# Kernel optimization log

Hardware: AMD Instinct MI355X
Metric: run time of the kernel (lower is better)

The kernel has to match this reference:

```python
import jax, jax.numpy as jnp
import numpy as np

SEQ, B, V, E, H, L = 64, 64, 32000, 512, 512, 2


def setup_inputs() -> dict:
    key = jax.random.key(0)
    ks = jax.random.split(key, 12)
    k = float(np.sqrt(1.0 / H))
    u = lambda kk, shape, a, b: jax.random.uniform(kk, shape, jnp.float32, a, b)
    return {
        "inputs": jax.random.randint(ks[0], (SEQ, B), 0, V),          # [T, B] token ids
        "hidden": jnp.zeros((L, B, H), jnp.float32),                   # initial hidden
        "emb": u(ks[1], (V, E), -0.1, 0.1),                            # embedding table
        "Wr_w": u(ks[2], (L, H, E + H), -k, k),                        # reset gate [L,H,2H]
        "Wr_b": u(ks[3], (L, H), -k, k),
        "Wz_w": u(ks[4], (L, H, E + H), -k, k),                        # update gate
        "Wz_b": u(ks[5], (L, H), -k, k),
        "Wh_w": u(ks[6], (L, H, E + H), -k, k),                        # candidate
        "Wh_b": u(ks[7], (L, H), -k, k),
        "out_w": u(ks[8], (V, H), -0.1, 0.1),                          # output projection
        "out_b": jnp.zeros((V,), jnp.float32),
    }


def reference(inputs, hidden, emb, Wr_w, Wr_b, Wz_w, Wz_b, Wh_w, Wh_b, out_w, out_b):
    # GRU recurrence over time via lax.scan (dropout disabled: dp_keep_prob=1.0)
    def step(h, tok):
        x = emb[tok]  # [B, E]
        new_h = []
        for i in range(L):  # fixed small layer loop
            hi = h[i]  # [B, H]
            cat = jnp.concatenate([x, hi], axis=1)  # [B, E+H]
            r = jax.nn.sigmoid(cat @ Wr_w[i].T + Wr_b[i])
            z = jax.nn.sigmoid(cat @ Wz_w[i].T + Wz_b[i])
            h_hat = jnp.tanh(jnp.concatenate([x, r * hi], axis=1) @ Wh_w[i].T + Wh_b[i])
            x = (1.0 - z) * hi + z * h_hat  # next layer input / new hidden
            new_h.append(x)
        logits_t = x @ out_w.T + out_b  # [B, V]
        return jnp.stack(new_h), logits_t

    hidden_final, logits = jax.lax.scan(step, hidden, inputs)
    return logits, hidden_final  # [T,B,V], [L,B,H]
```

## Files before the change

kernel.cpp:

```cpp
#include <hip/hip_runtime.h>

constexpr int NT = 64;
constexpr int NB = 64;
constexpr int NV = 32000;
constexpr int NE = 512;
constexpr int NH = 512;
constexpr int NTILE = 32 * 250;

constexpr size_t SZ_OW  = (size_t)NV * NE;
constexpr size_t SZ_XE  = (size_t)NT * NB * NE;
constexpr size_t SZ_H   = (size_t)NB * NH;
constexpr size_t LOGITS = (size_t)NT * NB * NV;

typedef float f32x4 __attribute__((ext_vector_type(4)));
typedef int   i32x4 __attribute__((ext_vector_type(4)));
typedef short bf16x8 __attribute__((ext_vector_type(8)));
typedef short s16x4 __attribute__((ext_vector_type(4)));
typedef _Float16 f16x8 __attribute__((ext_vector_type(8)));

__device__ __forceinline__ unsigned short f2bf(float x) {
  unsigned u = __float_as_uint(x);
  u += 0x7FFFu + ((u >> 16) & 1u);
  return (unsigned short)(u >> 16);
}
__device__ __forceinline__ float bf2f(unsigned short s) {
  return __uint_as_float(((unsigned)s) << 16);
}
__device__ __forceinline__ void split2(float v, short* hi, short* lo) {
  unsigned short h = f2bf(v);
  *hi = (short)h;
  *lo = (short)f2bf(v - bf2f(h));
}
__device__ __forceinline__ f32x4 mma_bf16(bf16x8 a, bf16x8 b, f32x4 c) {
  return __builtin_amdgcn_mfma_f32_16x16x32_bf16(a, b, c, 0, 0, 0);
}
__device__ __forceinline__ f32x4 mma_f16(f16x8 a, f16x8 b, f32x4 c) {
  return __builtin_amdgcn_mfma_f32_16x16x32_f16(a, b, c, 0, 0, 0);
}

__device__ __forceinline__ void st_sc32u(unsigned* p, unsigned v) {
  asm volatile("global_store_dword %0, %1, off sc0 sc1" :: "v"(p), "v"(v) : "memory");
}
__device__ __forceinline__ void st_sc128(void* p, i32x4 v) {
  asm volatile("global_store_dwordx4 %0, %1, off sc0 sc1" :: "v"(p), "v"(v) : "memory");
}
__device__ __forceinline__ void st_nt(float* p, float v) {
  asm volatile("global_store_dword %0, %1, off nt" :: "v"(p), "v"(v) : "memory");
}
__device__ __forceinline__ unsigned ld_sc32u(const unsigned* p) {
  unsigned v;
  asm volatile("global_load_dword %0, %1, off sc0 sc1\n\ts_waitcnt vmcnt(0)"
               : "=v"(v) : "v"(p) : "memory");
  return v;
}

__device__ __forceinline__ void publish(unsigned* flags, int slot, unsigned val) {
  asm volatile("s_waitcnt vmcnt(0)" ::: "memory");
  __syncthreads();
  if (threadIdx.x == 0) st_sc32u(&flags[(size_t)slot * 32], val);
}

__global__ void k_prep(
    const float* __restrict__ outw, const int* __restrict__ toks,
    const float* __restrict__ emb, const float* __restrict__ hid,
    _Float16* OWf, short* XeHi, short* XeLo,
    short* X1Hi, short* X1Lo, short* h0Hi, short* h0Lo) {
  const size_t stride = (size_t)gridDim.x * blockDim.x;
  const size_t N1 = SZ_OW, N2 = N1 + SZ_XE, N3 = N2 + SZ_H, N4 = N3 + SZ_H;
  for (size_t x = (size_t)blockIdx.x * blockDim.x + threadIdx.x; x < N4; x += stride) {
    if (x < N1) {
      OWf[x] = (_Float16)outw[x];
    } else if (x < N2) {
      size_t p = x - N1;
      size_t r = p >> 9, c = p & 511u;
      int tok = toks[r];
      float v = emb[(size_t)tok * 512 + c];
      short hi, lo; split2(v, &hi, &lo);
      XeHi[p] = hi; XeLo[p] = lo;
    } else if (x < N3) {
      size_t p = x - N2;
      short hi, lo; split2(hid[p], &hi, &lo);
      h0Hi[p] = hi; h0Lo[p] = lo;
    } else {
      size_t p = x - N3;
      short hi, lo; split2(hid[SZ_H + p], &hi, &lo);
      X1Hi[p] = hi; X1Lo[p] = lo;
    }
  }
}

__device__ __forceinline__ void mmaP32(
    const short* __restrict__ aH, const short* __restrict__ aL, int base,
    const short* lsHi_, const short* lsLo_,
    f32x4 (&accH)[2], f32x4 (&accL)[2], int wave, int l15, int lq) {
  const int kq = wave >> 1, rhalf = wave & 1;
  const int r0 = rhalf * 16 + l15;
#pragma unroll
  for (int i = 0; i < 4; ++i) {
    const int ko = kq * 128 + i * 32 + lq * 8;
    const int kg = base + ko;
    const int e0 = (l15 * 1024 + kg) ^ ((l15 & 7) << 3);
    const int e1 = ((16 + l15) * 1024 + kg) ^ ((l15 & 7) << 3);
    bf16x8 bh0 = *(const bf16x8*)&lsHi_[e0];
    bf16x8 bl0 = *(const bf16x8*)&lsLo_[e0];
    bf16x8 bh1 = *(const bf16x8*)&lsHi_[e1];
    bf16x8 bl1 = *(const bf16x8*)&lsLo_[e1];
    bf16x8 ah = *(const bf16x8*)&aH[r0 * 512 + ko];
    bf16x8 al = *(const bf16x8*)&aL[r0 * 512 + ko];
    accH[0] = mma_bf16(ah, bh0, accH[0]);
    accH[1] = mma_bf16(ah, bh1, accH[1]);
    accL[0] = mma_bf16(al, bh0, accL[0]);
    accL[1] = mma_bf16(al, bh1, accL[1]);
    accL[0] = mma_bf16(ah, bl0, accL[0]);
    accL[1] = mma_bf16(ah, bl1, accL[1]);
  }
}
__device__ __forceinline__ void reduce4(float* lsRed_, f32x4 (&accH)[2], f32x4 (&accL)[2],
                                        f32x4 (&acc)[2], int wave, int l15, int lq) {
  const int kq = wave >> 1, rhalf = wave & 1;
  acc[0] = accH[0] + accL[0];
  acc[1] = accH[1] + accL[1];
  const int pos = l15 * 16 + lq * 4;
  if (kq) {
    *(f32x4*)&lsRed_[(((kq - 1) * 2 + rhalf) * 2 + 0) * 256 + pos] = acc[0];
    *(f32x4*)&lsRed_[(((kq - 1) * 2 + rhalf) * 2 + 1) * 256 + pos] = acc[1];
  }
  __syncthreads();
  if (!kq) {
#pragma unroll
    for (int s = 0; s < 3; ++s) {
      acc[0] += *(const f32x4*)&lsRed_[((s * 2 + rhalf) * 2 + 0) * 256 + pos];
      acc[1] += *(const f32x4*)&lsRed_[((s * 2 + rhalf) * 2 + 1) * 256 + pos];
    }
  }
  __syncthreads();
}

__device__ __forceinline__ void mmaD(
    const short* __restrict__ pAH, const short* __restrict__ pAL,
    int kloc0, int kkGlob0, const short* lsHi_, const short* lsLo_,
    f32x4 (&accH)[2], f32x4 (&accL)[2], int l15, int lq, int rhalf, int rowbase) {
  const int r0 = rowbase + rhalf * 16 + l15;
#pragma unroll 4
  for (int i = 0; i < 8; ++i) {
    const int kk = kkGlob0 + i * 32 + lq * 8;
    const int ka = kloc0 + i * 32 + lq * 8;
    const int e0 = (l15 * 1024 + kk) ^ ((l15 & 7) << 3);
    const int e1 = ((16 + l15) * 1024 + kk) ^ ((l15 & 7) << 3);
    bf16x8 bh0 = *(const bf16x8*)&lsHi_[e0];
    bf16x8 bl0 = *(const bf16x8*)&lsLo_[e0];
    bf16x8 bh1 = *(const bf16x8*)&lsHi_[e1];
    bf16x8 bl1 = *(const bf16x8*)&lsLo_[e1];
    bf16x8 ah = *(const bf16x8*)&pAH[r0 * 512 + ka];
    bf16x8 al = *(const bf16x8*)&pAL[r0 * 512 + ka];
    accH[0] = mma_bf16(ah, bh0, accH[0]);
    accH[1] = mma_bf16(ah, bh1, accH[1]);
    accL[0] = mma_bf16(al, bh0, accL[0]);
    accL[1] = mma_bf16(al, bh1, accL[1]);
    accL[0] = mma_bf16(ah, bl0, accL[0]);
    accL[1] = mma_bf16(ah, bl1, accL[1]);
  }
}
__device__ __forceinline__ void phaseD(
    const short* aLoH, const short* aLoL,
    const short* aHiH, const short* aHiL,
    const short* lsHi_, const short* lsLo_, float* lsRed_,
    f32x4 (&acc)[2], int wave, int l15, int lq, int rowbase) {
  const int khalf = wave >> 1, rhalf = wave & 1;
  f32x4 accH[2] = {}, accL[2] = {};
  const short* pAH = (khalf < 2) ? aLoH : aHiH;
  const short* pAL = (khalf < 2) ? aLoL : aHiL;
  mmaD(pAH, pAL, (khalf & 1) * 256, khalf * 256, lsHi_, lsLo_,
       accH, accL, l15, lq, rhalf, rowbase);
  acc[0] = accH[0] + accL[0];
  acc[1] = accH[1] + accL[1];
  const int pos = l15 * 16 + lq * 4;
  if (wave >= 2) {
    *(f32x4*)&lsRed_[((wave - 2) * 2 + 0) * 256 + pos] = acc[0];
    *(f32x4*)&lsRed_[((wave - 2) * 2 + 1) * 256 + pos] = acc[1];
  }
  __syncthreads();
  if (wave < 2) {
#pragma unroll
    for (int s = 0; s < 3; ++s) {
      const int slot = (wave & 1) + 2 * s;
      acc[0] += *(const f32x4*)&lsRed_[(slot * 2 + 0) * 256 + pos];
      acc[1] += *(const f32x4*)&lsRed_[(slot * 2 + 1) * 256 + pos];
    }
  }
  __syncthreads();
}

__device__ __forceinline__ void stage_weights(
    short* lsHi, short* lsLo, const float* srcBase0, const float* srcBase1,
    int jc, int tid) {
  for (int i = tid; i < 8192; i += 512) {
    const int j = i >> 8;
    const int k4 = (i & 255) << 2;
    const int g = jc + j;
    const float* src = (srcBase1 && g >= 512)
        ? (srcBase1 + (size_t)(g - 512) * 1024 + k4)
        : (srcBase0 + (size_t)g * 1024 + k4);
    f32x4 v = *(const f32x4*)src;
    s16x4 h4, l4;
#pragma unroll
    for (int q = 0; q < 4; ++q) { short hi, lo; split2(v[q], &hi, &lo); h4[q] = hi; l4[q] = lo; }
    const int els = (j * 1024 + k4) ^ ((j & 7) << 3);
    *(s16x4*)&lsHi[els] = h4;
    *(s16x4*)&lsLo[els] = l4;
  }
}

__device__ void gemm_loop(char* pool, int tid,
                          const _Float16* Af, const _Float16* Bw,
                          const float* bias, float* C,
                          unsigned* flags, unsigned* tcnt) {
  _Float16* lsA = (_Float16*)pool;
  _Float16* lsB = lsA + 128 * 64;
  volatile int* bc = (volatile int*)(pool + 32768);
  const int wave = tid >> 6, lane = tid & 63, l15 = lane & 15, lq = lane >> 4;
  const int wr = (wave >> 2) * 64, wc = (wave & 3) * 32;
  unsigned lastR = 0;
  __syncthreads();
  for (;;) {
    if (tid == 0)
      *bc = (int)__hip_atomic_fetch_add(tcnt, 1u, __ATOMIC_RELAXED,
                                        __HIP_MEMORY_SCOPE_AGENT);
    __syncthreads();
    const int tau = *bc;
    __syncthreads();
    if (tau >= NTILE) break;
    const int bm = tau / 250, bn = tau - bm * 250;
    const unsigned Rneed = 2u * (unsigned)bm + 2u;
    if (lastR < Rneed) {
      if (tid < 32) {
        const unsigned* fp = &flags[(size_t)(160 + tid) * 32];
        while (ld_sc32u(fp) < Rneed) __builtin_amdgcn_s_sleep(8);
      }
      lastR = Rneed;
    }
    __syncthreads();
    f32x4 acc[4][2] = {};
    const size_t arow0 = (size_t)bm * 128;
    const size_t brow0 = (size_t)bn * 128;
    for (int kb = 0; kb < 512; kb += 64) {
#pragma unroll
      for (int i = 0; i < 2; ++i) {
        int c = tid + i * 512;
        int row = c >> 3, kc = (c & 7) * 8;
        f16x8 va = *(const f16x8*)(Af + (arow0 + row) * 512 + kb + kc);
        f16x8 vb = *(const f16x8*)(Bw + (brow0 + row) * 512 + kb + kc);
        int el = (row * 64 + kc) ^ ((row & 7) << 3);
        *(f16x8*)&lsA[el] = va;
        *(f16x8*)&lsB[el] = vb;
      }
      __syncthreads();
#pragma unroll
      for (int k0 = 0; k0 < 64; k0 += 32) {
        const int kk = k0 + lq * 8;
        f16x8 af[4], bfr[2];
#pragma unroll
        for (int i = 0; i < 4; ++i) {
          int ra = wr + i * 16 + l15;
          af[i] = *(const f16x8*)&lsA[(ra * 64 + kk) ^ ((ra & 7) << 3)];
        }
#pragma unroll
        for (int jt = 0; jt < 2; ++jt) {
          int rb = wc + jt * 16 + l15;
          bfr[jt] = *(const f16x8*)&lsB[(rb * 64 + kk) ^ ((rb & 7) << 3)];
        }
#pragma unroll
        for (int i = 0; i < 4; ++i)
#pragma unroll
          for (int jt = 0; jt < 2; ++jt)
            acc[i][jt] = mma_f16(af[i], bfr[jt], acc[i][jt]);
      }
      __syncthreads();
    }
#pragma unroll
    for (int i = 0; i < 4; ++i) {
#pragma unroll
      for (int jt = 0; jt < 2; ++jt) {
        const size_t col = brow0 + wc + jt * 16 + l15;
        const float bval = bias[col];
#pragma unroll
        for (int r = 0; r < 4; ++r) {
          const size_t row = arow0 + wr + i * 16 + lq * 4 + r;
          st_nt(&C[row * (size_t)NV + col], acc[i][jt][r] + bval);
        }
      }
    }
  }
}

__launch_bounds__(512, 1)
__global__ void k_main(
    const float* __restrict__ Wr, const float* __restrict__ Wz, const float* __restrict__ Wh,
    const float* __restrict__ Wrb, const float* __restrict__ Wzb, const float* __restrict__ Whb,
    const short* __restrict__ XeHi, const short* __restrict__ XeLo,
    short* X1Hi, short* X1Lo, _Float16* X1f16,
    short* h0Hi, short* h0Lo,
    short* rh0Hi, short* rh0Lo, short* rh1Hi, short* rh1Lo,
    float* z0, float* z1, float* hidOut,
    const _Float16* OWf, const float* outb, float* out,
    unsigned* flags, unsigned* tcnt) {
  __shared__ __align__(16) char pool[153600];
  short* lsHi = (short*)pool;
  short* lsLo = lsHi + 32 * 1024;
  float* lsRed = (float*)(pool + 131072);
  short* sH    = (short*)(pool + 131072);
  short* sL    = sH + 1024;
  float* sZA   = (float*)(pool + 131072);
  short* stH   = (short*)(pool + 143360);
  short* stL   = stH + 1024;
  float* sZ    = (float*)(pool + 147456);
  _Float16* sX = (_Float16*)(pool + 151552);

  const int wg = blockIdx.x;
  const int tid = threadIdx.x;
  const int wave = tid >> 6, lane = tid & 63, l15 = lane & 15, lq = lane >> 4;

  if (wg < 64) {
    const int cg = wg >> 1, rh = wg & 1, jc = cg * 32, rowbase = rh * 32;
    const bool isR = (jc < 512);
    stage_weights(lsHi, lsLo, Wr, Wz, jc, tid);
    float biasL0, biasL1;
    {
      const int j0 = jc + l15, j1 = j0 + 16;
      biasL0 = (j0 < 512) ? Wrb[j0] : Wzb[j0 - 512];
      biasL1 = (j1 < 512) ? Wrb[j1] : Wzb[j1 - 512];
    }
    __syncthreads();
    for (int t = 0; t < NT; ++t) {
      f32x4 accH[2] = {}, accL[2] = {};
      mmaP32(XeHi + (size_t)t * SZ_H + rowbase * 512,
             XeLo + (size_t)t * SZ_H + rowbase * 512, 0,
             lsHi, lsLo, accH, accL, wave, l15, lq);
      if (tid < 16) {
        const unsigned* fp = &flags[(size_t)(128 + tid * 2 + rh) * 32];
        while (ld_sc32u(fp) < (unsigned)t) {}
      }
      __syncthreads();
      const short* hH = h0Hi + (size_t)t * SZ_H + rowbase * 512;
      const short* hL = h0Lo + (size_t)t * SZ_H + rowbase * 512;
      if (isR && tid < 256) {
        const int buf = tid >> 7, q = tid & 127, row = q >> 2, c = q & 3;
        *(i32x4*)&(buf ? stL : stH)[row * 32 + c * 8] =
            *(const i32x4*)((buf ? hL : hH) + row * 512 + jc + c * 8);
      }
      mmaP32(hH, hL, 512, lsHi, lsLo, accH, accL, wave, l15, lq);
      f32x4 acc[2];
      reduce4(lsRed, accH, accL, acc, wave, l15, lq);
      if (wave < 2) {
#pragma unroll
        for (int ct = 0; ct < 2; ++ct) {
          const int jj = ct * 16 + l15;
          const float bv = ct ? biasL1 : biasL0;
#pragma unroll
          for (int r = 0; r < 4; ++r) {
            const int lb = wave * 16 + lq * 4 + r;
            const float s = 1.0f / (1.0f + __expf(-(acc[ct][r] + bv)));
            if (isR) {
              const float hv = bf2f((unsigned short)stH[lb * 32 + jj]) +
                               bf2f((unsigned short)stL[lb * 32 + jj]);
              short hi, lo; split2(s * hv, &hi, &lo);
              sH[lb * 32 + jj] = hi; sL[lb * 32 + jj] = lo;
            } else {
              sZA[lb * 32 + jj] = s;
            }
          }
        }
      }
      __syncthreads();
      if (isR) {
        if (tid < 256) {
          const int buf = tid >> 7, q = tid & 127, row = q >> 2, c = q & 3;
          i32x4 v = *(const i32x4*)&(buf ? sL : sH)[row * 32 + c * 8];
          st_sc128((buf ? rh0Lo : rh0Hi) + (size_t)t * SZ_H +
                   (size_t)(rowbase + row) * 512 + jc + c * 8, v);
        }
      } else {
        if (tid < 256) {
          const int row = tid >> 3, c = tid & 7;
          i32x4 v = *(const i32x4*)&sZA[row * 32 + c * 4];
          st_sc128(z0 + (size_t)t * SZ_H + (size_t)(rowbase + row) * 512 +
                   (jc - 512) + c * 4, v);
        }
      }
      publish(flags, wg, (unsigned)(t + 1));
    }
  } else if (wg < 128) {
    const int idx = wg - 64, cg = idx >> 1, rh = idx & 1, jc = cg * 32, rowbase = rh * 32;
    const bool isR = (jc < 512);
    stage_weights(lsHi, lsLo, Wr + (size_t)512 * 1024, Wz + (size_t)512 * 1024, jc, tid);
    float biasL0, biasL1;
    {
      const int j0 = jc + l15, j1 = j0 + 16;
      biasL0 = (j0 < 512) ? Wrb[512 + j0] : Wzb[512 + j0 - 512];
      biasL1 = (j1 < 512) ? Wrb[512 + j1] : Wzb[512 + j1 - 512];
    }
    __syncthreads();
    for (int t = 0; t < NT; ++t) {
      if (tid < 16) {
        const unsigned* fp = &flags[(size_t)(128 + tid * 2 + rh) * 32];
        while (ld_sc32u(fp) < (unsigned)(t + 1)) {}
      } else if (tid >= 64 && tid < 80) {
        const unsigned* fp = &flags[(size_t)(160 + (tid - 64) * 2 + rh) * 32];
        while (ld_sc32u(fp) < (unsigned)t) {}
      }
      __syncthreads();
      const short* xH = h0Hi + (size_t)(t + 1) * SZ_H;
      const short* xL = h0Lo + (size_t)(t + 1) * SZ_H;
      const short* hH = X1Hi + (size_t)t * SZ_H;
      const short* hL = X1Lo + (size_t)t * SZ_H;
      if (isR && tid < 256) {
        const int buf = tid >> 7, q = tid & 127, row = q >> 2, c = q & 3;
        *(i32x4*)&(buf ? stL : stH)[row * 32 + c * 8] =
            *(const i32x4*)((buf ? hL : hH) + (size_t)(rowbase + row) * 512 + jc + c * 8);
      }
      f32x4 acc[2];
      phaseD(xH, xL, hH, hL, lsHi, lsLo, lsRed, acc, wave, l15, lq, rowbase);
      if (wave < 2) {
#pragma unroll
        for (int ct = 0; ct < 2; ++ct) {
          const int jj = ct * 16 + l15;
          const float bv = ct ? biasL1 : biasL0;
#pragma unroll
          for (int r = 0; r < 4; ++r) {
            const int lb = wave * 16 + lq * 4 + r;
            const float s = 1.0f / (1.0f + __expf(-(acc[ct][r] + bv)));
            if (isR) {
              const float hv = bf2f((unsigned short)stH[lb * 32 + jj]) +
                               bf2f((unsigned short)stL[lb * 32 + jj]);
              short hi, lo; split2(s * hv, &hi, &lo);
              sH[lb * 32 + jj] = hi; sL[lb * 32 + jj] = lo;
            } else {
              sZA[lb * 32 + jj] = s;
            }
          }
        }
      }
      __syncthreads();
      if (isR) {
        if (tid < 256) {
          const int buf = tid >> 7, q = tid & 127, row = q >> 2, c = q & 3;
          i32x4 v = *(const i32x4*)&(buf ? sL : sH)[row * 32 + c * 8];
          st_sc128((buf ? rh1Lo : rh1Hi) + (size_t)t * SZ_H +
                   (size_t)(rowbase + row) * 512 + jc + c * 8, v);
        }
      } else {
        if (tid < 256) {
          const int row = tid >> 3, c = tid & 7;
          i32x4 v = *(const i32x4*)&sZA[row * 32 + c * 4];
          st_sc128(z1 + (size_t)t * SZ_H + (size_t)(rowbase + row) * 512 +
                   (jc - 512) + c * 4, v);
        }
      }
      publish(flags, wg, (unsigned)(t + 1));
    }
  } else if (wg < 192) {
    const bool isL1 = (wg >= 160);
    const int idx = isL1 ? (wg - 160) : (wg - 128);
    const int cg = idx >> 1, rh = idx & 1, jc = cg * 32, rowbase = rh * 32;
    const int layer = isL1 ? 1 : 0;
    stage_weights(lsHi, lsLo, Wh + (size_t)layer * 512 * 1024, nullptr, jc, tid);
    const float biasL0 = Whb[layer * 512 + jc + l15];
    const float biasL1 = Whb[layer * 512 + jc + 16 + l15];
    __syncthreads();
    short* myHi = isL1 ? X1Hi : h0Hi;
    short* myLo = isL1 ? X1Lo : h0Lo;
    const short* rhHi_ = isL1 ? rh1Hi : rh0Hi;
    const short* rhLo_ = isL1 ? rh1Lo : rh0Lo;
    const float* zArr = isL1 ? z1 : z0;
    for (int t = 0; t < NT; ++t) {
      if (tid < 256) {
        const int buf = tid >> 7, q = tid & 127, row = q >> 2, c = q & 3;
        const short* src = (buf ? myLo : myHi) + (size_t)t * SZ_H +
                           (size_t)(rowbase + row) * 512 + jc + c * 8;
        *(i32x4*)&(buf ? stL : stH)[row * 32 + c * 8] = *(const i32x4*)src;
      }
      if (isL1) {
        if (tid < 16) {
          const unsigned* fp = &flags[(size_t)(128 + tid * 2 + rh) * 32];
          while (ld_sc32u(fp) < (unsigned)(t + 1)) {}
        }
        __syncthreads();
      }
      f32x4 accH[2] = {}, accL[2] = {};
      if (isL1) {
        mmaP32(h0Hi + (size_t)(t + 1) * SZ_H + rowbase * 512,
               h0Lo + (size_t)(t + 1) * SZ_H + rowbase * 512, 0,
               lsHi, lsLo, accH, accL, wave, l15, lq);
      } else {
        mmaP32(XeHi + (size_t)t * SZ_H + rowbase * 512,
               XeLo + (size_t)t * SZ_H + rowbase * 512, 0,
               lsHi, lsLo, accH, accL, wave, l15, lq);
      }
      if (tid < 32) {
        const int base = isL1 ? 64 : 0;
        const unsigned* fp = &flags[(size_t)(base + tid * 2 + rh) * 32];
        while (ld_sc32u(fp) < (unsigned)(t + 1)) {}
      }
      __syncthreads();
      if (tid < 256) {
        const int row = tid >> 3, c = tid & 7;
        *(f32x4*)&sZ[row * 32 + c * 4] =
            *(const f32x4*)(zArr + (size_t)t * SZ_H + (size_t)(rowbase + row) * 512 +
                            jc + c * 4);
      }
      mmaP32(rhHi_ + (size_t)t * SZ_H + rowbase * 512,
             rhLo_ + (size_t)t * SZ_H + rowbase * 512, 512,
             lsHi, lsLo, accH, accL, wave, l15, lq);
      f32x4 acc[2];
      reduce4(lsRed, accH, accL, acc, wave, l15, lq);
      if (wave < 2) {
#pragma unroll
        for (int ct = 0; ct < 2; ++ct) {
          const int jj = ct * 16 + l15, j = jc + jj;
          const float bv = ct ? biasL1 : biasL0;
#pragma unroll
          for (int r = 0; r < 4; ++r) {
            const int lb = wave * 16 + lq * 4 + r;
            const float hh = tanhf(acc[ct][r] + bv);
            const float z = sZ[lb * 32 + jj];
            const float ho = bf2f((unsigned short)stH[lb * 32 + jj]) +
                             bf2f((unsigned short)stL[lb * 32 + jj]);
            const float hn = (1.0f - z) * ho + z * hh;
            short hi, lo; split2(hn, &hi, &lo);
            sH[lb * 32 + jj] = hi; sL[lb * 32 + jj] = lo;
            if (isL1) sX[lb * 32 + jj] = (_Float16)hn;
            if (t == NT - 1)
              hidOut[(size_t)layer * SZ_H + (size_t)(rowbase + lb) * 512 + j] = hn;
          }
        }
      }
      __syncthreads();
      if (tid < 256) {
        const int buf = tid >> 7, q = tid & 127, row = q >> 2, c = q & 3;
        i32x4 v = *(const i32x4*)&(buf ? sL : sH)[row * 32 + c * 8];
        st_sc128((buf ? myLo : myHi) + (size_t)(t + 1) * SZ_H +
                 (size_t)(rowbase + row) * 512 + jc + c * 8, v);
      } else if (isL1 && tid < 384) {
        const int q = tid - 256, row = q >> 2, c = q & 3;
        i32x4 v = *(const i32x4*)&sX[row * 32 + c * 8];
        st_sc128(X1f16 + (size_t)t * SZ_H + (size_t)(rowbase + row) * 512 + jc + c * 8, v);
      }
      publish(flags, wg, (unsigned)(t + 1));
    }
  }
  {
    unsigned* tc = tcnt;
    gemm_loop(pool, tid, X1f16, OWf, outb, out, flags, tc);
  }
}

extern "C" void kernel_launch(void* const* d_in, const int* in_sizes, int n_in,
                              void* d_out, int out_size, void* d_ws, size_t ws_size,
                              hipStream_t stream) {
  (void)in_sizes; (void)n_in; (void)out_size; (void)ws_size;
  const int*   toks = (const int*)d_in[0];
  const float* hid  = (const float*)d_in[1];
  const float* emb  = (const float*)d_in[2];
  const float* Wr   = (const float*)d_in[3];
  const float* Wrb  = (const float*)d_in[4];
  const float* Wz   = (const float*)d_in[5];
  const float* Wzb  = (const float*)d_in[6];
  const float* Wh   = (const float*)d_in[7];
  const float* Whb  = (const float*)d_in[8];
  const float* outw = (const float*)d_in[9];
  const float* outb = (const float*)d_in[10];
  float* out = (float*)d_out;

  char* base = (char*)d_ws;
  size_t off = 0;
  auto carve = [&](size_t bytes) -> char* {
    char* r = base + off;
    off = (off + bytes + 255) & ~(size_t)255;
    return r;
  };
  _Float16* OWf   = (_Float16*)carve(SZ_OW * 2);
  short*    XeHi  = (short*)carve(SZ_XE * 2);
  short*    XeLo  = (short*)carve(SZ_XE * 2);
  short*    X1Hi  = (short*)carve((size_t)(NT + 1) * SZ_H * 2);
  short*    X1Lo  = (short*)carve((size_t)(NT + 1) * SZ_H * 2);
  _Float16* X1f16 = (_Float16*)carve((size_t)NT * SZ_H * 2);
  short*    h0Hi  = (short*)carve((size_t)(NT + 1) * SZ_H * 2);
  short*    h0Lo  = (short*)carve((size_t)(NT + 1) * SZ_H * 2);
  short*    rh0Hi = (short*)carve((size_t)NT * SZ_H * 2);
  short*    rh0Lo = (short*)carve((size_t)NT * SZ_H * 2);
  short*    rh1Hi = (short*)carve((size_t)NT * SZ_H * 2);
  short*    rh1Lo = (short*)carve((size_t)NT * SZ_H * 2);
  float*    z0    = (float*)carve((size_t)NT * SZ_H * 4);
  float*    z1    = (float*)carve((size_t)NT * SZ_H * 4);
  unsigned* flags = (unsigned*)carve(32768);
  unsigned* tcnt  = (unsigned*)carve(256);

  hipMemsetAsync(flags, 0, 32768, stream);
  hipMemsetAsync(tcnt, 0, 256, stream);

  k_prep<<<2048, 256, 0, stream>>>(outw, toks, emb, hid,
                                   OWf, XeHi, XeLo, X1Hi, X1Lo, h0Hi, h0Lo);

  k_main<<<256, 512, 0, stream>>>(
      Wr, Wz, Wh, Wrb, Wzb, Whb, XeHi, XeLo,
      X1Hi, X1Lo, X1f16, h0Hi, h0Lo,
      rh0Hi, rh0Lo, rh1Hi, rh1Lo, z0, z1,
      out + LOGITS, OWf, outb, out, flags, tcnt);
}
```

Measured before the change: 790.9 us.

## Keep A tile resident in LDS across five N tiles and split recurrence flag waits

The output-projection GEMM loop now claims chunks of five N tiles per M block. It stages the full 128x512 f16 A tile into LDS once per block row and reuses it, so only B is streamed per k-step. In the recurrent phases, flag waits are split so each wave waits only for the part of the h state it is about to multiply, which lets more MMA work overlap with other workgroups' progress. The larger LDS footprint and coarser work chunks may reduce load balance, and the finer flag-wait ordering depends on the producers' publish layout being correct.

```diff
diff --git a/kernel.cpp b/kernel.cpp
--- a/kernel.cpp
+++ b/kernel.cpp
@@ -5,7 +5,7 @@
 constexpr int NV = 32000;
 constexpr int NE = 512;
 constexpr int NH = 512;
-constexpr int NTILE = 32 * 250;
+constexpr int NCHUNK = 32 * 50;
 
 constexpr size_t SZ_OW  = (size_t)NV * NE;
 constexpr size_t SZ_XE  = (size_t)NT * NB * NE;
@@ -136,61 +136,6 @@
   __syncthreads();
 }
 
-__device__ __forceinline__ void mmaD(
-    const short* __restrict__ pAH, const short* __restrict__ pAL,
-    int kloc0, int kkGlob0, const short* lsHi_, const short* lsLo_,
-    f32x4 (&accH)[2], f32x4 (&accL)[2], int l15, int lq, int rhalf, int rowbase) {
-  const int r0 = rowbase + rhalf * 16 + l15;
-#pragma unroll 4
-  for (int i = 0; i < 8; ++i) {
-    const int kk = kkGlob0 + i * 32 + lq * 8;
-    const int ka = kloc0 + i * 32 + lq * 8;
-    const int e0 = (l15 * 1024 + kk) ^ ((l15 & 7) << 3);
-    const int e1 = ((16 + l15) * 1024 + kk) ^ ((l15 & 7) << 3);
-    bf16x8 bh0 = *(const bf16x8*)&lsHi_[e0];
-    bf16x8 bl0 = *(const bf16x8*)&lsLo_[e0];
-    bf16x8 bh1 = *(const bf16x8*)&lsHi_[e1];
-    bf16x8 bl1 = *(const bf16x8*)&lsLo_[e1];
-    bf16x8 ah = *(const bf16x8*)&pAH[r0 * 512 + ka];
-    bf16x8 al = *(const bf16x8*)&pAL[r0 * 512 + ka];
-    accH[0] = mma_bf16(ah, bh0, accH[0]);
-    accH[1] = mma_bf16(ah, bh1, accH[1]);
-    accL[0] = mma_bf16(al, bh0, accL[0]);
-    accL[1] = mma_bf16(al, bh1, accL[1]);
-    accL[0] = mma_bf16(ah, bl0, accL[0]);
-    accL[1] = mma_bf16(ah, bl1, accL[1]);
-  }
-}
-__device__ __forceinline__ void phaseD(
-    const short* aLoH, const short* aLoL,
-    const short* aHiH, const short* aHiL,
-    const short* lsHi_, const short* lsLo_, float* lsRed_,
-    f32x4 (&acc)[2], int wave, int l15, int lq, int rowbase) {
-  const int khalf = wave >> 1, rhalf = wave & 1;
-  f32x4 accH[2] = {}, accL[2] = {};
-  const short* pAH = (khalf < 2) ? aLoH : aHiH;
-  const short* pAL = (khalf < 2) ? aLoL : aHiL;
-  mmaD(pAH, pAL, (khalf & 1) * 256, khalf * 256, lsHi_, lsLo_,
-       accH, accL, l15, lq, rhalf, rowbase);
-  acc[0] = accH[0] + accL[0];
-  acc[1] = accH[1] + accL[1];
-  const int pos = l15 * 16 + lq * 4;
-  if (wave >= 2) {
-    *(f32x4*)&lsRed_[((wave - 2) * 2 + 0) * 256 + pos] = acc[0];
-    *(f32x4*)&lsRed_[((wave - 2) * 2 + 1) * 256 + pos] = acc[1];
-  }
-  __syncthreads();
-  if (wave < 2) {
-#pragma unroll
-    for (int s = 0; s < 3; ++s) {
-      const int slot = (wave & 1) + 2 * s;
-      acc[0] += *(const f32x4*)&lsRed_[(slot * 2 + 0) * 256 + pos];
-      acc[1] += *(const f32x4*)&lsRed_[(slot * 2 + 1) * 256 + pos];
-    }
-  }
-  __syncthreads();
-}
-
 __device__ __forceinline__ void stage_weights(
     short* lsHi, short* lsLo, const float* srcBase0, const float* srcBase1,
     int jc, int tid) {
@@ -216,21 +161,22 @@
                           const float* bias, float* C,
                           unsigned* flags, unsigned* tcnt) {
   _Float16* lsA = (_Float16*)pool;
-  _Float16* lsB = lsA + 128 * 64;
-  volatile int* bc = (volatile int*)(pool + 32768);
+  _Float16* lsB = (_Float16*)(pool + 131072);
+  volatile int* bc = (volatile int*)(pool + 147456);
   const int wave = tid >> 6, lane = tid & 63, l15 = lane & 15, lq = lane >> 4;
   const int wr = (wave >> 2) * 64, wc = (wave & 3) * 32;
   unsigned lastR = 0;
+  int lastBm = -1;
   __syncthreads();
   for (;;) {
     if (tid == 0)
       *bc = (int)__hip_atomic_fetch_add(tcnt, 1u, __ATOMIC_RELAXED,
                                         __HIP_MEMORY_SCOPE_AGENT);
     __syncthreads();
-    const int tau = *bc;
+    const int chunk = *bc;
     __syncthreads();
-    if (tau >= NTILE) break;
-    const int bm = tau / 250, bn = tau - bm * 250;
+    if (chunk >= NCHUNK) break;
+    const int bm = chunk / 50, bn0 = (chunk - bm * 50) * 5;
     const unsigned Rneed = 2u * (unsigned)bm + 2u;
     if (lastR < Rneed) {
       if (tid < 32) {
@@ -238,55 +184,67 @@
         while (ld_sc32u(fp) < Rneed) __builtin_amdgcn_s_sleep(8);
       }
       lastR = Rneed;
-    }
-    __syncthreads();
-    f32x4 acc[4][2] = {};
+      __syncthreads();
+    }
+    if (bm != lastBm) {
+      __syncthreads();
+      const size_t arow0 = (size_t)bm * 128;
+#pragma unroll
+      for (int i = 0; i < 16; ++i) {
+        int c = tid + i * 512;
+        int row = c >> 6, kc = (c & 63) * 8;
+        f16x8 va = *(const f16x8*)(Af + (arow0 + row) * 512 + kc);
+        *(f16x8*)&lsA[(row * 512 + kc) ^ ((row & 7) << 3)] = va;
+      }
+      lastBm = bm;
+      __syncthreads();
+    }
     const size_t arow0 = (size_t)bm * 128;
-    const size_t brow0 = (size_t)bn * 128;
-    for (int kb = 0; kb < 512; kb += 64) {
-#pragma unroll
-      for (int i = 0; i < 2; ++i) {
-        int c = tid + i * 512;
-        int row = c >> 3, kc = (c & 7) * 8;
-        f16x8 va = *(const f16x8*)(Af + (arow0 + row) * 512 + kb + kc);
-        f16x8 vb = *(const f16x8*)(Bw + (brow0 + row) * 512 + kb + kc);
-        int el = (row * 64 + kc) ^ ((row & 7) << 3);
-        *(f16x8*)&lsA[el] = va;
-        *(f16x8*)&lsB[el] = vb;
-      }
-      __syncthreads();
-#pragma unroll
-      for (int k0 = 0; k0 < 64; k0 += 32) {
-        const int kk = k0 + lq * 8;
-        f16x8 af[4], bfr[2];
-#pragma unroll
-        for (int i = 0; i < 4; ++i) {
-          int ra = wr + i * 16 + l15;
-          af[i] = *(const f16x8*)&lsA[(ra * 64 + kk) ^ ((ra & 7) << 3)];
-        }
+    for (int bn = bn0; bn < bn0 + 5; ++bn) {
+      const size_t brow0 = (size_t)bn * 128;
+      f32x4 acc[4][2] = {};
+      for (int kb = 0; kb < 512; kb += 64) {
+#pragma unroll
+        for (int i = 0; i < 2; ++i) {
+          int c = tid + i * 512;
+          int row = c >> 3, kc = (c & 7) * 8;
+          f16x8 vb = *(const f16x8*)(Bw + (brow0 + row) * 512 + kb + kc);
+          *(f16x8*)&lsB[(row * 64 + kc) ^ ((row & 7) << 3)] = vb;
+        }
+        __syncthreads();
+#pragma unroll
+        for (int k0 = 0; k0 < 64; k0 += 32) {
+          const int kk = k0 + lq * 8;
+          f16x8 af[4], bfr[2];
+#pragma unroll
+          for (int i = 0; i < 4; ++i) {
+            int ra = wr + i * 16 + l15;
+            af[i] = *(const f16x8*)&lsA[(ra * 512 + kb + kk) ^ ((ra & 7) << 3)];
+          }
+#pragma unroll
+          for (int jt = 0; jt < 2; ++jt) {
+            int rb = wc + jt * 16 + l15;
+            bfr[jt] = *(const f16x8*)&lsB[(rb * 64 + kk) ^ ((rb & 7) << 3)];
+          }
+#pragma unroll
+          for (int i = 0; i < 4; ++i)
+#pragma unroll
+            for (int jt = 0; jt < 2; ++jt)
+              acc[i][jt] = mma_f16(af[i], bfr[jt], acc[i][jt]);
+        }
+        __syncthreads();
+      }
+#pragma unroll
+      for (int i = 0; i < 4; ++i) {
 #pragma unroll
         for (int jt = 0; jt < 2; ++jt) {
-          int rb = wc + jt * 16 + l15;
-          bfr[jt] = *(const f16x8*)&lsB[(rb * 64 + kk) ^ ((rb & 7) << 3)];
-        }
-#pragma unroll
-        for (int i = 0; i < 4; ++i)
-#pragma unroll
-          for (int jt = 0; jt < 2; ++jt)
-            acc[i][jt] = mma_f16(af[i], bfr[jt], acc[i][jt]);
-      }
-      __syncthreads();
-    }
-#pragma unroll
-    for (int i = 0; i < 4; ++i) {
-#pragma unroll
-      for (int jt = 0; jt < 2; ++jt) {
-        const size_t col = brow0 + wc + jt * 16 + l15;
-        const float bval = bias[col];
-#pragma unroll
-        for (int r = 0; r < 4; ++r) {
-          const size_t row = arow0 + wr + i * 16 + lq * 4 + r;
-          st_nt(&C[row * (size_t)NV + col], acc[i][jt][r] + bval);
+          const size_t col = brow0 + wc + jt * 16 + l15;
+          const float bval = bias[col];
+#pragma unroll
+          for (int r = 0; r < 4; ++r) {
+            const size_t row = arow0 + wr + i * 16 + lq * 4 + r;
+            st_nt(&C[row * (size_t)NV + col], acc[i][jt][r] + bval);
+          }
         }
       }
     }
@@ -343,12 +301,12 @@
       __syncthreads();
       const short* hH = h0Hi + (size_t)t * SZ_H + rowbase * 512;
       const short* hL = h0Lo + (size_t)t * SZ_H + rowbase * 512;
+      mmaP32(hH, hL, 512, lsHi, lsLo, accH, accL, wave, l15, lq);
       if (isR && tid < 256) {
         const int buf = tid >> 7, q = tid & 127, row = q >> 2, c = q & 3;
         *(i32x4*)&(buf ? stL : stH)[row * 32 + c * 8] =
             *(const i32x4*)((buf ? hL : hH) + row * 512 + jc + c * 8);
       }
-      mmaP32(hH, hL, 512, lsHi, lsLo, accH, accL, wave, l15, lq);
       f32x4 acc[2];
       reduce4(lsRed, accH, accL, acc, wave, l15, lq);
       if (wave < 2) {
@@ -402,24 +360,29 @@
     __syncthreads();
     for (int t = 0; t < NT; ++t) {
       if (tid < 16) {
+        const unsigned* fp = &flags[(size_t)(160 + tid * 2 + rh) * 32];
+        while (ld_sc32u(fp) < (unsigned)t) {}
+      }
+      __syncthreads();
+      const short* hH = X1Hi + (size_t)t * SZ_H + rowbase * 512;
+      const short* hL = X1Lo + (size_t)t * SZ_H + rowbase * 512;
+      f32x4 accH[2] = {}, accL[2] = {};
+      mmaP32(hH, hL, 512, lsHi, lsLo, accH, accL, wave, l15, lq);
+      if (tid < 16) {
         const unsigned* fp = &flags[(size_t)(128 + tid * 2 + rh) * 32];
         while (ld_sc32u(fp) < (unsigned)(t + 1)) {}
-      } else if (tid >= 64 && tid < 80) {
-        const unsigned* fp = &flags[(size_t)(160 + (tid - 64) * 2 + rh) * 32];
-        while (ld_sc32u(fp) < (unsigned)t) {}
-      }
-      __syncthreads();
-      const short* xH = h0Hi + (size_t)(t + 1) * SZ_H;
-      const short* xL = h0Lo + (size_t)(t + 1) * SZ_H;
-      const short* hH = X1Hi + (size_t)t * SZ_H;
-      const short* hL = X1Lo + (size_t)t * SZ_H;
+      }
+      __syncthreads();
+      mmaP32(h0Hi + (size_t)(t + 1) * SZ_H + rowbase * 512,
+             h0Lo + (size_t)(t + 1) * SZ_H + rowbase * 512, 0,
+             lsHi, lsLo, accH, accL, wave, l15, lq);
       if (isR && tid < 256) {
         const int buf = tid >> 7, q = tid & 127, row = q >> 2, c = q & 3;
         *(i32x4*)&(buf ? stL : stH)[row * 32 + c * 8] =
-            *(const i32x4*)((buf ? hL : hH) + (size_t)(rowbase + row) * 512 + jc + c * 8);
+            *(const i32x4*)((buf ? hL : hH) + row * 512 + jc + c * 8);
       }
       f32x4 acc[2];
-      phaseD(xH, xL, hH, hL, lsHi, lsLo, lsRed, acc, wave, l15, lq, rowbase);
+      reduce4(lsRed, accH, accL, acc, wave, l15, lq);
       if (wave < 2) {
 #pragma unroll
         for (int ct = 0; ct < 2; ++ct) {
@@ -472,6 +435,7 @@
     const short* rhHi_ = isL1 ? rh1Hi : rh0Hi;
     const short* rhLo_ = isL1 ? rh1Lo : rh0Lo;
     const float* zArr = isL1 ? z1 : z0;
+    const int fbase = isL1 ? 64 : 0;
     for (int t = 0; t < NT; ++t) {
       if (tid < 256) {
         const int buf = tid >> 7, q = tid & 127, row = q >> 2, c = q & 3;
@@ -479,15 +443,13 @@
                            (size_t)(rowbase + row) * 512 + jc + c * 8;
         *(i32x4*)&(buf ? stL : stH)[row * 32 + c * 8] = *(const i32x4*)src;
       }
+      f32x4 accH[2] = {}, accL[2] = {};
       if (isL1) {
         if (tid < 16) {
           const unsigned* fp = &flags[(size_t)(128 + tid * 2 + rh) * 32];
           while (ld_sc32u(fp) < (unsigned)(t + 1)) {}
         }
         __syncthreads();
-      }
-      f32x4 accH[2] = {}, accL[2] = {};
-      if (isL1) {
         mmaP32(h0Hi + (size_t)(t + 1) * SZ_H + rowbase * 512,
                h0Lo + (size_t)(t + 1) * SZ_H + rowbase * 512, 0,
                lsHi, lsLo, accH, accL, wave, l15, lq);
@@ -496,9 +458,16 @@
                XeLo + (size_t)t * SZ_H + rowbase * 512, 0,
                lsHi, lsLo, accH, accL, wave, l15, lq);
       }
-      if (tid < 32) {
-        const int base = isL1 ? 64 : 0;
-        const unsigned* fp = &flags[(size_t)(base + tid * 2 + rh) * 32];
+      if (tid < 16) {
+        const unsigned* fp = &flags[(size_t)(fbase + tid * 2 + rh) * 32];
+        while (ld_sc32u(fp) < (unsigned)(t + 1)) {}
+      }
+      __syncthreads();
+      mmaP32(rhHi_ + (size_t)t * SZ_H + rowbase * 512,
+             rhLo_ + (size_t)t * SZ_H + rowbase * 512, 512,
+             lsHi, lsLo, accH, accL, wave, l15, lq);
+      if (tid < 16) {
+        const unsigned* fp = &flags[(size_t)(fbase + (16 + tid) * 2 + rh) * 32];
         while (ld_sc32u(fp) < (unsigned)(t + 1)) {}
       }
       __syncthreads();
@@ -508,9 +477,6 @@
             *(const f32x4*)(zArr + (size_t)t * SZ_H + (size_t)(rowbase + row) * 512 +
                             jc + c * 4);
       }
-      mmaP32(rhHi_ + (size_t)t * SZ_H + rowbase * 512,
-             rhLo_ + (size_t)t * SZ_H + rowbase * 512, 512,
-             lsHi, lsLo, accH, accL, wave, l15, lq);
       f32x4 acc[2];
       reduce4(lsRed, accH, accL, acc, wave, l15, lq);
       if (wave < 2) {
@@ -548,10 +514,7 @@
       publish(flags, wg, (unsigned)(t + 1));
     }
   }
-  {
-    unsigned* tc = tcnt;
-    gemm_loop(pool, tid, X1f16, OWf, outb, out, flags, tc);
-  }
+  gemm_loop(pool, tid, X1f16, OWf, outb, out, flags, tcnt);
 }
 
 extern "C" void kernel_launch(void* const* d_in, const int* in_sizes, int n_in,
```

Measured after the change: 891.4 us. +12.7%, slower.
